# Kernel tuning notes

Measured on AMD Instinct MI355X. Metric: run time of the kernel, lower is better.

## Reference

```python
import jax, jax.numpy as jnp
import numpy as np

N = 50000      # nodes
E = 800000     # edges
G = 512        # graphs in batch
F0 = 92        # orig atom feature len
F = 64         # atom_fea_len
NB = 41        # nbr_fea_len
H = 128        # h_fea_len
NCONV = 3
EPS = 1e-5


def setup_inputs() -> dict:
    key = jax.random.key(0)
    ks = jax.random.split(key, 16)
    s = 0.05
    inp = {
        "x": jax.random.normal(ks[0], (N, F0), jnp.float32),
        "edge_index": jax.random.randint(ks[1], (2, E), 0, N),
        "edge_attr": jax.random.normal(ks[2], (E, NB), jnp.float32),
        "batch": jnp.sort(jax.random.randint(ks[3], (N,), 0, G)),
        # embedding (only applied at the first conv, when x width == F0)
        "emb_W": jax.random.normal(ks[4], (F0, F), jnp.float32) * s,
        "emb_b": jnp.zeros((F,), jnp.float32),
        # per-conv-layer params, stacked on leading axis
        "bn1_g": jnp.ones((NCONV, F), jnp.float32),
        "bn1_b": jnp.zeros((NCONV, F), jnp.float32),
        "bn2_g": jnp.ones((NCONV, F), jnp.float32),
        "bn2_b": jnp.zeros((NCONV, F), jnp.float32),
        "lnf_W": jax.random.normal(ks[5], (NCONV, 2 * F + NB, F), jnp.float32) * s,
        "lnf_b": jnp.zeros((NCONV, F), jnp.float32),
        "lns_W": jax.random.normal(ks[6], (NCONV, 2 * F + NB, F), jnp.float32) * s,
        "lns_b": jnp.zeros((NCONV, F), jnp.float32),
        # readout MLP
        "fc1_W": jax.random.normal(ks[7], (F, H), jnp.float32) * s,
        "fc1_b": jnp.zeros((H,), jnp.float32),
        "out_W": jax.random.normal(ks[8], (H, 1), jnp.float32) * s,
        "out_b": jnp.zeros((1,), jnp.float32),
    }
    return inp


def _batchnorm(x, g, b):
    # training-mode BatchNorm1d: batch stats over node dim, biased variance
    mean = jnp.mean(x, axis=0)
    var = jnp.var(x, axis=0)
    return (x - mean) * jax.lax.rsqrt(var + EPS) * g + b


def _cgconv(x, edge_index, edge_attr, bn1_g, bn1_b, bn2_g, bn2_b, Wf, bf, Ws, bs):
    x = _batchnorm(x, bn1_g, bn1_b)
    # flow='target_to_source': x_i = x[edge_index[0]], x_j = x[edge_index[1]],
    # aggregation scatter-adds messages to edge_index[0]
    src, dst = edge_index[0], edge_index[1]
    z = jnp.concatenate([x[src], x[dst], edge_attr], axis=-1)   # [E, 2F+NB]
    m = jax.nn.sigmoid(z @ Wf + bf) * jax.nn.softplus(z @ Ws + bs)
    agg = jax.ops.segment_sum(m, src, num_segments=x.shape[0])  # [N, F]
    out = _batchnorm(agg, bn2_g, bn2_b) + x
    return jax.nn.softplus(out)


def reference(x, edge_index, edge_attr, batch, emb_W, emb_b,
              bn1_g, bn1_b, bn2_g, bn2_b, lnf_W, lnf_b, lns_W, lns_b,
              fc1_W, fc1_b, out_W, out_b):
    h = x @ emb_W + emb_b  # first conv applies embedding (x width == F0)
    for i in range(NCONV):
        h = _cgconv(h, edge_index, edge_attr,
                    bn1_g[i], bn1_b[i], bn2_g[i], bn2_b[i],
                    lnf_W[i], lnf_b[i], lns_W[i], lns_b[i])
    # global mean pool per graph
    sums = jax.ops.segment_sum(h, batch, num_segments=G)
    cnts = jax.ops.segment_sum(jnp.ones((h.shape[0], 1), h.dtype), batch, num_segments=G)
    crys = sums / jnp.maximum(cnts, 1.0)                         # [G, F]
    crys = jax.nn.softplus(jax.nn.softplus(crys) @ fc1_W + fc1_b)
    return crys @ out_W + out_b                                  # [G, 1]
```

## Files before the change

kernel.cpp:

```cpp
#include <hip/hip_runtime.h>
#include <hip/hip_bf16.h>

#define NN 50000
#define NE 800000
#define NG 512
#define F0 92
#define FF 64
#define NB 41
#define HH 128
#define NBLK_SCAN 196
#define NBATCH (NE / 64)
#define WBSZ (2 * 8 * 64 * 8)
#define PACK_EB 128

typedef __attribute__((ext_vector_type(4))) float f32x4;
typedef __attribute__((ext_vector_type(8))) short bf16x8;

__device__ __forceinline__ float softplusf(float x) {
    return fmaxf(x, 0.f) + __logf(1.f + __expf(-fabsf(x)));
}
__device__ __forceinline__ float sigmoidf(float x) {
    return __fdividef(1.f, 1.f + __expf(-x));
}
__device__ __forceinline__ ushort f2bf(float v) {
    __hip_bfloat16 b = __float2bfloat16(v);
    return *reinterpret_cast<ushort*>(&b);
}


__global__ __launch_bounds__(256) void hist_kernel(const int* __restrict__ ei,
                                                   int* __restrict__ cnt)
{
    for (int e = blockIdx.x * 256 + threadIdx.x; e < NE; e += gridDim.x * 256)
        atomicAdd(&cnt[ei[e]], 1);
}

__global__ __launch_bounds__(256) void scan1_kernel(const int* __restrict__ cnt,
                                                    int* __restrict__ bsum)
{
    __shared__ int sd[256];
    const int t = threadIdx.x;
    const int idx = blockIdx.x * 256 + t;
    sd[t] = (idx < NN) ? cnt[idx] : 0;
    __syncthreads();
    for (int s = 128; s > 0; s >>= 1) {
        if (t < s) sd[t] += sd[t + s];
        __syncthreads();
    }
    if (t == 0) bsum[blockIdx.x] = sd[0];
}

__global__ __launch_bounds__(256) void scan2_kernel(int* __restrict__ bsum)
{
    __shared__ int sd[256];
    const int t = threadIdx.x;
    const int v = (t < NBLK_SCAN) ? bsum[t] : 0;
    sd[t] = v;
    __syncthreads();
    for (int off = 1; off < 256; off <<= 1) {
        int a = (t >= off) ? sd[t - off] : 0;
        __syncthreads();
        sd[t] += a;
        __syncthreads();
    }
    if (t < NBLK_SCAN) bsum[t] = sd[t] - v;
}

__global__ __launch_bounds__(256) void scan3_kernel(const int* __restrict__ cnt,
                                                    const int* __restrict__ bsum,
                                                    int* __restrict__ cursor)
{
    __shared__ int sd[256];
    const int t = threadIdx.x;
    const int idx = blockIdx.x * 256 + t;
    const int v = (idx < NN) ? cnt[idx] : 0;
    sd[t] = v;
    __syncthreads();
    for (int off = 1; off < 256; off <<= 1) {
        int a = (t >= off) ? sd[t - off] : 0;
        __syncthreads();
        sd[t] += a;
        __syncthreads();
    }
    if (idx < NN) cursor[idx] = bsum[blockIdx.x] + sd[t] - v;
}

__global__ __launch_bounds__(256) void scatter_kernel(const int* __restrict__ ei,
                                                      int* __restrict__ cursor,
                                                      int4* __restrict__ esd)
{
    for (int e = blockIdx.x * 256 + threadIdx.x; e < NE; e += gridDim.x * 256) {
        const int s = ei[e];
        const int d = ei[NE + e];
        const int pos = atomicAdd(&cursor[s], 1);
        esd[pos] = make_int4(e, s, d, 0);
    }
}

__global__ __launch_bounds__(128) void pack_kernel(const float* __restrict__ ea,
                                                   ushort* __restrict__ eaP)
{
    __shared__ float rowbuf[PACK_EB * NB];
    const int t = threadIdx.x;
    const size_t base = (size_t)blockIdx.x * PACK_EB;
    const float* src = ea + base * NB;
    for (int i = t; i < PACK_EB * NB; i += 128) rowbuf[i] = src[i];
    __syncthreads();
    uint* out = (uint*)eaP + base * 32;
#pragma unroll
    for (int i = 0; i < 32; ++i) {
        const int idx = i * 128 + t;
        const int e = idx >> 5, k2 = (idx & 31) * 2;
        const float v0 = (k2 < NB) ? rowbuf[e * NB + k2] : 0.f;
        const float v1 = (k2 + 1 < NB) ? rowbuf[e * NB + k2 + 1] : 0.f;
        out[idx] = (uint)f2bf(v0) | ((uint)f2bf(v1) << 16);
    }
}

__global__ __launch_bounds__(256) void prep_kernel(
    const float* __restrict__ lnfW, const float* __restrict__ lnsW,
    ushort* __restrict__ wB)
{
    const int total = 3 * WBSZ;
    for (int idx = blockIdx.x * 256 + threadIdx.x; idx < total; idx += gridDim.x * 256) {
        const int j = idx & 7;
        const int lane = (idx >> 3) & 63;
        const int nt = (idx >> 9) & 7;
        const int t2 = (idx >> 12) & 1;
        const int i = idx >> 13;
        const int k = t2 * 32 + (lane >> 4) * 8 + j;
        const int col = (nt & 3) * 16 + (lane & 15);
        const float* W = (nt < 4 ? lnfW : lnsW) + (size_t)i * 169 * FF;
        wB[idx] = (k < NB) ? f2bf(W[(2 * FF + k) * FF + col]) : (ushort)0;
    }
}


__global__ __launch_bounds__(256) void emb_kernel(
    const float* __restrict__ x, const float* __restrict__ W,
    const float* __restrict__ bias, float* __restrict__ h,
    float* __restrict__ stats0)
{
    __shared__ float sx[4][F0];
    __shared__ float sdr[2][4][FF];
    const int lane = threadIdx.x & 63;
    const int w = threadIdx.x >> 6;
    float wr[F0];
#pragma unroll
    for (int k = 0; k < F0; ++k) wr[k] = W[k * FF + lane];
    const float bv = bias[lane];
    float s = 0.f, s2 = 0.f;
    const int nit = NN / 4;
    for (int it = blockIdx.x; it < nit; it += gridDim.x) {
        const int n = it * 4 + w;
        if (lane < 46) {
            sx[w][lane * 2]     = x[n * F0 + lane * 2];
            sx[w][lane * 2 + 1] = x[n * F0 + lane * 2 + 1];
        }
        __syncthreads();
        float acc = bv;
#pragma unroll
        for (int k4 = 0; k4 < F0 / 4; ++k4) {
            float4 q = *(const float4*)&sx[w][k4 * 4];
            acc = fmaf(q.x, wr[k4 * 4 + 0], acc);
            acc = fmaf(q.y, wr[k4 * 4 + 1], acc);
            acc = fmaf(q.z, wr[k4 * 4 + 2], acc);
            acc = fmaf(q.w, wr[k4 * 4 + 3], acc);
        }
        h[n * FF + lane] = acc;
        s += acc;
        s2 = fmaf(acc, acc, s2);
        __syncthreads();
    }
    sdr[0][w][lane] = s;
    sdr[1][w][lane] = s2;
    __syncthreads();
    if (threadIdx.x < FF) {
        const int f = threadIdx.x;
        atomicAdd(&stats0[f],      sdr[0][0][f] + sdr[0][1][f] + sdr[0][2][f] + sdr[0][3][f]);
        atomicAdd(&stats0[FF + f], sdr[1][0][f] + sdr[1][1][f] + sdr[1][2][f] + sdr[1][3][f]);
    }
}

__global__ __launch_bounds__(256) void stats_kernel(
    const float* __restrict__ src, float* __restrict__ stats)
{
    __shared__ float sd[2][4][FF];
    const int f = threadIdx.x & 63;
    const int r = threadIdx.x >> 6;
    float s = 0.f, s2 = 0.f;
    for (int n = blockIdx.x * 4 + r; n < NN; n += gridDim.x * 4) {
        float v = src[n * FF + f];
        s += v;
        s2 = fmaf(v, v, s2);
    }
    sd[0][r][f] = s;
    sd[1][r][f] = s2;
    __syncthreads();
    if (threadIdx.x < FF) {
        atomicAdd(&stats[f],      sd[0][0][f] + sd[0][1][f] + sd[0][2][f] + sd[0][3][f]);
        atomicAdd(&stats[FF + f], sd[1][0][f] + sd[1][1][f] + sd[1][2][f] + sd[1][3][f]);
    }
}

__global__ __launch_bounds__(256) void node_kernel(
    const float* __restrict__ h, const float* __restrict__ stats,
    const float* __restrict__ gbn, const float* __restrict__ bbn,
    const float* __restrict__ Wf, const float* __restrict__ Ws,
    const float* __restrict__ bf, const float* __restrict__ bs,
    float* __restrict__ xn, float* __restrict__ pS, float* __restrict__ pD)
{
    __shared__ float sx[4][FF];
    const int lane = threadIdx.x & 63;
    const int w = threadIdx.x >> 6;
    const float* W = (w < 2) ? Wf : Ws;
    const int rowbase = (w & 1) * FF;
    float wr[FF];
#pragma unroll
    for (int k = 0; k < FF; ++k) wr[k] = W[(rowbase + k) * FF + lane];
    const float inv = 1.f / (float)NN;
    const float mean = stats[lane] * inv;
    const float var = stats[FF + lane] * inv - mean * mean;
    const float A = rsqrtf(var + 1e-5f) * gbn[lane];
    const float B = fmaf(-mean, A, bbn[lane]);
    float bias = 0.f;
    if (w == 0) bias = bf[lane];
    if (w == 2) bias = bs[lane];
    float* outp = ((w & 1) ? pD : pS) + ((w >> 1) & 1);
    for (int n = blockIdx.x; n < NN; n += gridDim.x) {
        const float xv = fmaf(h[n * FF + lane], A, B);
        if (w == 0) xn[n * FF + lane] = xv;
        sx[w][lane] = xv;
        __syncthreads();
        float acc = bias;
#pragma unroll
        for (int k4 = 0; k4 < FF / 4; ++k4) {
            float4 q = *(const float4*)&sx[w][k4 * 4];
            acc = fmaf(q.x, wr[k4 * 4 + 0], acc);
            acc = fmaf(q.y, wr[k4 * 4 + 1], acc);
            acc = fmaf(q.z, wr[k4 * 4 + 2], acc);
            acc = fmaf(q.w, wr[k4 * 4 + 3], acc);
        }
        outp[(size_t)n * 128 + 2 * lane] = acc;
        __syncthreads();
    }
}

__global__ __launch_bounds__(256)
void edge_kernel(const ushort* __restrict__ eaP, const int4* __restrict__ esd,
                 const ushort* __restrict__ wB,
                 const float* __restrict__ pS, const float* __restrict__ pD,
                 float* __restrict__ agg)
{
    __shared__ ushort wlds[WBSZ];
    const int t = threadIdx.x, lane = t & 63;
    for (int i = t; i < WBSZ / 8; i += 256)
        ((int4*)wlds)[i] = ((const int4*)wB)[i];
    __syncthreads();
    const int le = lane >> 4, lf = lane & 15;
    const int nw = (gridDim.x * 256) >> 6;
    const int gw = (blockIdx.x * 256 + t) >> 6;

    for (int b = gw; b < NBATCH; b += nw) {
        const int4 rec = esd[b * 64 + lane];
#pragma unroll 1
        for (int g = 0; g < 4; ++g) {
            const int eg  = __shfl(rec.x, g * 16 + lf, 64);
            const int sv0 = __shfl(rec.y, g * 16 + le * 4 + 0, 64);
            const int sv1 = __shfl(rec.y, g * 16 + le * 4 + 1, 64);
            const int sv2 = __shfl(rec.y, g * 16 + le * 4 + 2, 64);
            const int sv3 = __shfl(rec.y, g * 16 + le * 4 + 3, 64);
            const int dv0 = __shfl(rec.z, g * 16 + le * 4 + 0, 64);
            const int dv1 = __shfl(rec.z, g * 16 + le * 4 + 1, 64);
            const int dv2 = __shfl(rec.z, g * 16 + le * 4 + 2, 64);
            const int dv3 = __shfl(rec.z, g * 16 + le * 4 + 3, 64);
            const bf16x8 af0 = *(const bf16x8*)&eaP[(size_t)eg * 64 + le * 8];
            const bf16x8 af1 = *(const bf16x8*)&eaP[(size_t)eg * 64 + 32 + le * 8];
#pragma unroll 1
            for (int p = 0; p < 4; ++p) {
                const bf16x8 bG0 = *(const bf16x8*)&wlds[((0 * 8 + p) * 64 + lane) * 8];
                const bf16x8 bG1 = *(const bf16x8*)&wlds[((1 * 8 + p) * 64 + lane) * 8];
                const bf16x8 bC0 = *(const bf16x8*)&wlds[((0 * 8 + p + 4) * 64 + lane) * 8];
                const bf16x8 bC1 = *(const bf16x8*)&wlds[((1 * 8 + p + 4) * 64 + lane) * 8];
                f32x4 aG = {0.f, 0.f, 0.f, 0.f}, aC = {0.f, 0.f, 0.f, 0.f};
                aG = __builtin_amdgcn_mfma_f32_16x16x32_bf16(af0, bG0, aG, 0, 0, 0);
                aG = __builtin_amdgcn_mfma_f32_16x16x32_bf16(af1, bG1, aG, 0, 0, 0);
                aC = __builtin_amdgcn_mfma_f32_16x16x32_bf16(af0, bC0, aC, 0, 0, 0);
                aC = __builtin_amdgcn_mfma_f32_16x16x32_bf16(af1, bC1, aC, 0, 0, 0);
                const int fo = 2 * (p * 16 + lf);
                const float2 s20 = *(const float2*)(pS + (size_t)sv0 * 128 + fo);
                const float2 d20 = *(const float2*)(pD + (size_t)dv0 * 128 + fo);
                const float2 s21 = *(const float2*)(pS + (size_t)sv1 * 128 + fo);
                const float2 d21 = *(const float2*)(pD + (size_t)dv1 * 128 + fo);
                const float2 s22 = *(const float2*)(pS + (size_t)sv2 * 128 + fo);
                const float2 d22 = *(const float2*)(pD + (size_t)dv2 * 128 + fo);
                const float2 s23 = *(const float2*)(pS + (size_t)sv3 * 128 + fo);
                const float2 d23 = *(const float2*)(pD + (size_t)dv3 * 128 + fo);
                const float m0 = sigmoidf(aG[0] + s20.x + d20.x) * softplusf(aC[0] + s20.y + d20.y);
                const float m1 = sigmoidf(aG[1] + s21.x + d21.x) * softplusf(aC[1] + s21.y + d21.y);
                const float m2 = sigmoidf(aG[2] + s22.x + d22.x) * softplusf(aC[2] + s22.y + d22.y);
                const float m3 = sigmoidf(aG[3] + s23.x + d23.x) * softplusf(aC[3] + s23.y + d23.y);
                const int fcol = p * 16 + lf;
                float run = m0;
                if (sv1 == sv0) run += m1;
                else { unsafeAtomicAdd(&agg[(size_t)sv0 * FF + fcol], run); run = m1; }
                if (sv2 == sv1) run += m2;
                else { unsafeAtomicAdd(&agg[(size_t)sv1 * FF + fcol], run); run = m2; }
                if (sv3 == sv2) run += m3;
                else { unsafeAtomicAdd(&agg[(size_t)sv2 * FF + fcol], run); run = m3; }
                unsafeAtomicAdd(&agg[(size_t)sv3 * FF + fcol], run);
            }
        }
    }
}

__global__ __launch_bounds__(256) void update_kernel(
    const float* __restrict__ agg, const float* __restrict__ xn,
    const float* __restrict__ stats,
    const float* __restrict__ gbn, const float* __restrict__ bbn,
    float* __restrict__ h, const int* __restrict__ batch,
    float* __restrict__ pool, float* __restrict__ pcnt,
    float* __restrict__ statsNext, const int do_pool)
{
    __shared__ float sdr[2][4][FF];
    const int myf = threadIdx.x & 63;
    const float inv = 1.f / (float)NN;
    const float mean = stats[myf] * inv;
    const float var = stats[FF + myf] * inv - mean * mean;
    const float A = rsqrtf(var + 1e-5f) * gbn[myf];
    const float B = fmaf(-mean, A, bbn[myf]);
    float s = 0.f, s2 = 0.f;
    const int total = NN * FF;
    for (int idx = blockIdx.x * blockDim.x + threadIdx.x; idx < total;
         idx += gridDim.x * blockDim.x) {
        const int n = idx >> 6;
        const float v = softplusf(fmaf(agg[idx], A, B) + xn[idx]);
        if (do_pool) {
            const int g = batch[n];
            unsafeAtomicAdd(&pool[g * FF + myf], v);
            if (myf == 0) unsafeAtomicAdd(&pcnt[g], 1.f);
        } else {
            h[idx] = v;
            s += v;
            s2 = fmaf(v, v, s2);
        }
    }
    if (!do_pool) {
        const int r = threadIdx.x >> 6;
        sdr[0][r][myf] = s;
        sdr[1][r][myf] = s2;
        __syncthreads();
        if (threadIdx.x < FF) {
            atomicAdd(&statsNext[myf],      sdr[0][0][myf] + sdr[0][1][myf] + sdr[0][2][myf] + sdr[0][3][myf]);
            atomicAdd(&statsNext[FF + myf], sdr[1][0][myf] + sdr[1][1][myf] + sdr[1][2][myf] + sdr[1][3][myf]);
        }
    }
}

__global__ __launch_bounds__(128) void readout_kernel(
    const float* __restrict__ pool, const float* __restrict__ pcnt,
    const float* __restrict__ fc1W, const float* __restrict__ fc1b,
    const float* __restrict__ outW, const float* __restrict__ outb,
    float* __restrict__ out)
{
    __shared__ float sp[FF];
    __shared__ float red[2];
    const int g = blockIdx.x;
    const int t = threadIdx.x;
    if (t < FF) {
        const float c = fmaxf(pcnt[g], 1.f);
        sp[t] = softplusf(pool[g * FF + t] / c);
    }
    __syncthreads();
    float a = fc1b[t];
#pragma unroll
    for (int k = 0; k < FF; ++k) a = fmaf(sp[k], fc1W[k * HH + t], a);
    float o = softplusf(a) * outW[t];
#pragma unroll
    for (int off = 32; off > 0; off >>= 1) o += __shfl_down(o, off, 64);
    if ((t & 63) == 0) red[t >> 6] = o;
    __syncthreads();
    if (t == 0) out[g] = red[0] + red[1] + outb[0];
}

extern "C" void kernel_launch(void* const* d_in, const int* in_sizes, int n_in,
                              void* d_out, int out_size, void* d_ws, size_t ws_size,
                              hipStream_t stream)
{
    const float* x     = (const float*)d_in[0];
    const int*   ei    = (const int*)  d_in[1];
    const float* ea    = (const float*)d_in[2];
    const int*   batch = (const int*)  d_in[3];
    const float* embW  = (const float*)d_in[4];
    const float* embb  = (const float*)d_in[5];
    const float* bn1g  = (const float*)d_in[6];
    const float* bn1b  = (const float*)d_in[7];
    const float* bn2g  = (const float*)d_in[8];
    const float* bn2b  = (const float*)d_in[9];
    const float* lnfW  = (const float*)d_in[10];
    const float* lnfb  = (const float*)d_in[11];
    const float* lnsW  = (const float*)d_in[12];
    const float* lnsb  = (const float*)d_in[13];
    const float* fc1W  = (const float*)d_in[14];
    const float* fc1b  = (const float*)d_in[15];
    const float* outW  = (const float*)d_in[16];
    const float* outb  = (const float*)d_in[17];

    float* ws      = (float*)d_ws;
    float* h       = ws;
    float* xn      = h   + (size_t)NN * FF;
    float* pS      = xn  + (size_t)NN * FF;
    float* pD      = pS  + (size_t)NN * 128;
    float* agg     = pD  + (size_t)NN * 128;
    float* pool    = agg + (size_t)NN * FF;
    float* pcnt    = pool + (size_t)NG * FF;
    float* statsB1 = pcnt + NG;
    float* statsB2 = statsB1 + 3 * 256;
    int*   cnt     = (int*)(statsB2 + 3 * 256);
    int*   cursor  = cnt + NN;
    int*   bsum    = cursor + NN;
    int4*  esd     = (int4*)(bsum + 256);
    ushort* wB     = (ushort*)(esd + NE);
    ushort* eaP    = wB + 3 * WBSZ;

    hipMemsetAsync(cnt, 0, NN * sizeof(int), stream);
    hipMemsetAsync(pool, 0, (NG * FF + NG + 6 * 256) * sizeof(float), stream);

    hist_kernel<<<2048, 256, 0, stream>>>(ei, cnt);
    scan1_kernel<<<NBLK_SCAN, 256, 0, stream>>>(cnt, bsum);
    scan2_kernel<<<1, 256, 0, stream>>>(bsum);
    scan3_kernel<<<NBLK_SCAN, 256, 0, stream>>>(cnt, bsum, cursor);
    scatter_kernel<<<2048, 256, 0, stream>>>(ei, cursor, esd);
    pack_kernel<<<NE / PACK_EB, 128, 0, stream>>>(ea, eaP);
    prep_kernel<<<96, 256, 0, stream>>>(lnfW, lnsW, wB);
    emb_kernel<<<1024, 256, 0, stream>>>(x, embW, embb, h, statsB1);

    for (int i = 0; i < 3; ++i) {
        const float* Wf  = lnfW + (size_t)i * 169 * FF;
        const float* Wsp = lnsW + (size_t)i * 169 * FF;
        float* s1 = statsB1 + (size_t)i * 256;
        float* s2 = statsB2 + (size_t)i * 256;
        node_kernel<<<1024, 256, 0, stream>>>(h, s1, bn1g + i * FF, bn1b + i * FF,
                                              Wf, Wsp, lnfb + i * FF, lnsb + i * FF,
                                              xn, pS, pD);
        hipMemsetAsync(agg, 0, (size_t)NN * FF * sizeof(float), stream);
        edge_kernel<<<2048, 256, 0, stream>>>(eaP, esd, wB + (size_t)i * WBSZ,
                                              pS, pD, agg);
        stats_kernel<<<256, 256, 0, stream>>>(agg, s2);
        update_kernel<<<2048, 256, 0, stream>>>(agg, xn, s2, bn2g + i * FF, bn2b + i * FF,
                                                h, batch, pool, pcnt,
                                                statsB1 + (size_t)(i + 1 < 3 ? i + 1 : 0) * 256,
                                                (i == 2) ? 1 : 0);
    }
    readout_kernel<<<NG, HH, 0, stream>>>(pool, pcnt, fc1W, fc1b, outW, outb, (float*)d_out);
}
```

Baseline: 1.057 ms.

## Pack edge attributes in sorted-edge order and MFMA fragment layout

The pack kernel now gathers edge attribute rows through the sorted edge permutation and writes them already arranged in the per-lane MFMA A-fragment order. The edge kernel then reads each fragment with fully contiguous, coalesced loads instead of gathering scattered rows by original edge id three times, once per conv layer. The cost moves to a single scattered gather in the pack kernel, which now also depends on the scatter kernel's output.

```diff
diff --git a/kernel.cpp b/kernel.cpp
--- a/kernel.cpp
+++ b/kernel.cpp
@@ -98,22 +98,30 @@
 }
 
 __global__ __launch_bounds__(128) void pack_kernel(const float* __restrict__ ea,
+                                                   const int4* __restrict__ esd,
                                                    ushort* __restrict__ eaP)
 {
     __shared__ float rowbuf[PACK_EB * NB];
+    __shared__ int eid[PACK_EB];
     const int t = threadIdx.x;
     const size_t base = (size_t)blockIdx.x * PACK_EB;
-    const float* src = ea + base * NB;
-    for (int i = t; i < PACK_EB * NB; i += 128) rowbuf[i] = src[i];
+    eid[t] = esd[base + t].x;
+    __syncthreads();
+    for (int i = t; i < PACK_EB * NB; i += 128) {
+        const int e = i / NB, k = i - e * NB;
+        rowbuf[i] = ea[(size_t)eid[e] * NB + k];
+    }
     __syncthreads();
     uint* out = (uint*)eaP + base * 32;
-#pragma unroll
-    for (int i = 0; i < 32; ++i) {
-        const int idx = i * 128 + t;
-        const int e = idx >> 5, k2 = (idx & 31) * 2;
-        const float v0 = (k2 < NB) ? rowbuf[e * NB + k2] : 0.f;
-        const float v1 = (k2 + 1 < NB) ? rowbuf[e * NB + k2 + 1] : 0.f;
-        out[idx] = (uint)f2bf(v0) | ((uint)f2bf(v1) << 16);
+    for (int i = t; i < PACK_EB * 32; i += 128) {
+        const int gg = i >> 9;
+        const int r = i & 511;
+        const int t2 = r >> 8, lg = (r >> 6) & 3, rw = (r >> 2) & 15, ju = r & 3;
+        const int e = gg * 16 + rw;
+        const int k = t2 * 32 + lg * 8 + ju * 2;
+        const float v0 = (k < NB) ? rowbuf[e * NB + k] : 0.f;
+        const float v1 = (k + 1 < NB) ? rowbuf[e * NB + k + 1] : 0.f;
+        out[i] = (uint)f2bf(v0) | ((uint)f2bf(v1) << 16);
     }
 }
 
@@ -265,7 +273,8 @@
         const int4 rec = esd[b * 64 + lane];
 #pragma unroll 1
         for (int g = 0; g < 4; ++g) {
-            const int eg  = __shfl(rec.x, g * 16 + lf, 64);
+            const bf16x8 af0 = *(const bf16x8*)&eaP[(((size_t)(b * 4 + g) * 2 + 0) * 64 + lane) * 8];
+            const bf16x8 af1 = *(const bf16x8*)&eaP[(((size_t)(b * 4 + g) * 2 + 1) * 64 + lane) * 8];
             const int sv0 = __shfl(rec.y, g * 16 + le * 4 + 0, 64);
             const int sv1 = __shfl(rec.y, g * 16 + le * 4 + 1, 64);
             const int sv2 = __shfl(rec.y, g * 16 + le * 4 + 2, 64);
@@ -274,8 +283,6 @@
             const int dv1 = __shfl(rec.z, g * 16 + le * 4 + 1, 64);
             const int dv2 = __shfl(rec.z, g * 16 + le * 4 + 2, 64);
             const int dv3 = __shfl(rec.z, g * 16 + le * 4 + 3, 64);
-            const bf16x8 af0 = *(const bf16x8*)&eaP[(size_t)eg * 64 + le * 8];
-            const bf16x8 af1 = *(const bf16x8*)&eaP[(size_t)eg * 64 + 32 + le * 8];
 #pragma unroll 1
             for (int p = 0; p < 4; ++p) {
                 const bf16x8 bG0 = *(const bf16x8*)&wlds[((0 * 8 + p) * 64 + lane) * 8];
@@ -431,7 +438,7 @@
     scan2_kernel<<<1, 256, 0, stream>>>(bsum);
     scan3_kernel<<<NBLK_SCAN, 256, 0, stream>>>(cnt, bsum, cursor);
     scatter_kernel<<<2048, 256, 0, stream>>>(ei, cursor, esd);
-    pack_kernel<<<NE / PACK_EB, 128, 0, stream>>>(ea, eaP);
+    pack_kernel<<<NE / PACK_EB, 128, 0, stream>>>(ea, esd, eaP);
     prep_kernel<<<96, 256, 0, stream>>>(lnfW, lnsW, wB);
     emb_kernel<<<1024, 256, 0, stream>>>(x, embW, embb, h, statsB1);
 
```

After: 1.066 ms. No clear change (+0.9%).
